# Kernel tuning notes

Hardware: AMD Instinct MI355X
Metric: run time of the kernel (lower is better)

The kernel has to match this reference:

```python
import jax, jax.numpy as jnp
import numpy as np

B, L, H = 32, 1024, 384


def setup_inputs() -> dict:
    key = jax.random.key(0)
    k1, k2 = jax.random.split(key)
    encoder_hidden_states = jax.random.normal(k1, (B, L, H), dtype=jnp.float32)
    durations_gt = jax.random.randint(k2, (B, L), 0, 8, dtype=jnp.int32)
    return {"encoder_hidden_states": encoder_hidden_states, "durations_gt": durations_gt}


def reference(encoder_hidden_states, durations_gt):
    # cumulative end-frame of each phoneme: [B, L]
    cum = jnp.cumsum(durations_gt, axis=1)
    total = cum[:, -1]                      # [B] expanded length per batch item
    T = int(jnp.max(total))                 # max expanded length (data-dependent)
    t = jnp.arange(T, dtype=cum.dtype)      # [T] output frame positions
    # source phoneme index for each output frame: number of cum entries <= t
    idx = jax.vmap(lambda c: jnp.searchsorted(c, t, side="right"))(cum)  # [B, T]
    idx = jnp.minimum(idx, L - 1)
    mask = (t[None, :] < total[:, None]).astype(jnp.float32)             # [B, T]
    # gather hidden states and zero out the padded tail
    out = jnp.take_along_axis(encoder_hidden_states, idx[:, :, None], axis=1)
    out = out * mask[:, :, None]
    return out, mask
```

## Files before the change

### kernel.cpp

```cpp
#include <hip/hip_runtime.h>

#define BB 32
#define LL 1024
#define HH 384
#define H4 (HH / 4)
#define TT 64
#define NT 256

__global__ __launch_bounds__(NT) void lenreg_kernel(
    const float* __restrict__ ehs,
    const int* __restrict__ dur,
    float* __restrict__ out,
    float* __restrict__ mask,
    int T)
{
    __shared__ int scum[LL];
    __shared__ int psum[NT];
    __shared__ int sidx[TT];

    const int tid = threadIdx.x;
    const int b   = blockIdx.y;
    const int t0  = blockIdx.x * TT;

    int4 d = ((const int4*)(dur + (size_t)b * LL))[tid];
    int p0 = d.x;
    int p1 = p0 + d.y;
    int p2 = p1 + d.z;
    int p3 = p2 + d.w;
    psum[tid] = p3;
    __syncthreads();
    #pragma unroll
    for (int off = 1; off < NT; off <<= 1) {
        int v = (tid >= off) ? psum[tid - off] : 0;
        __syncthreads();
        psum[tid] += v;
        __syncthreads();
    }
    const int excl = (tid > 0) ? psum[tid - 1] : 0;
    scum[4 * tid + 0] = excl + p0;
    scum[4 * tid + 1] = excl + p1;
    scum[4 * tid + 2] = excl + p2;
    scum[4 * tid + 3] = excl + p3;
    __syncthreads();

    const int total = scum[LL - 1];

    if (tid < TT) {
        const int t = t0 + tid;
        int lo = 0, hi = LL;
        while (lo < hi) {
            const int mid = (lo + hi) >> 1;
            if (scum[mid] <= t) lo = mid + 1; else hi = mid;
        }
        sidx[tid] = (lo < LL - 1) ? lo : (LL - 1);
        if (t < T) mask[(size_t)b * T + t] = (t < total) ? 1.0f : 0.0f;
    }
    __syncthreads();

    const float4* __restrict__ src_base = (const float4*)(ehs + (size_t)b * LL * HH);
    float4* __restrict__ out4 = (float4*)out;
    const float4 zero4 = make_float4(0.f, 0.f, 0.f, 0.f);

    for (int w = tid; w < TT * H4; w += NT) {
        const int tl = w / H4;
        const int v  = w - tl * H4;
        const int t  = t0 + tl;
        if (t >= T) break;
        float4 val = zero4;
        if (t < total) {
            val = src_base[(size_t)sidx[tl] * H4 + v];
        }
        out4[((size_t)b * T + t) * H4 + v] = val;
    }
}

extern "C" void kernel_launch(void* const* d_in, const int* in_sizes, int n_in,
                              void* d_out, int out_size, void* d_ws, size_t ws_size,
                              hipStream_t stream) {
    const float* ehs = (const float*)d_in[0];
    const int*   dur = (const int*)d_in[1];

    const int T = out_size / (BB * (HH + 1));

    float* out  = (float*)d_out;
    float* mask = (float*)d_out + (size_t)BB * T * HH;

    dim3 grid((T + TT - 1) / TT, BB);
    dim3 block(NT);
    lenreg_kernel<<<grid, block, 0, stream>>>(ehs, dur, out, mask, T);
}
```

Measured before the change: 229.2 us.

## Split prefix scan into separate kernel and double frames per block

Moves the per-batch cumulative sum of durations into a small pre-pass kernel that writes the scan to workspace. The gather blocks then load the precomputed cumulative array instead of redoing the scan in every block. The frame tile per block is also doubled, so there are fewer blocks and each one does more copying. The cost is an extra kernel launch and a global round-trip for the cumulative array.

```diff
diff --git a/kernel.cpp b/kernel.cpp
--- a/kernel.cpp
+++ b/kernel.cpp
@@ -4,43 +4,55 @@
 #define LL 1024
 #define HH 384
 #define H4 (HH / 4)
-#define TT 64
+#define TT 128
 #define NT 256
 
-__global__ __launch_bounds__(NT) void lenreg_kernel(
+__global__ __launch_bounds__(NT) void scan_kernel(
+    const int* __restrict__ dur,
+    int* __restrict__ cum)
+{
+    __shared__ int psum[NT];
+    const int tid = threadIdx.x;
+    const int b   = blockIdx.x;
+
+    int4 d = ((const int4*)(dur + (size_t)b * LL))[tid];
+    const int p0 = d.x;
+    const int p1 = p0 + d.y;
+    const int p2 = p1 + d.z;
+    const int p3 = p2 + d.w;
+    psum[tid] = p3;
+    __syncthreads();
+    #pragma unroll
+    for (int off = 1; off < NT; off <<= 1) {
+        const int v = (tid >= off) ? psum[tid - off] : 0;
+        __syncthreads();
+        psum[tid] += v;
+        __syncthreads();
+    }
+    const int excl = (tid > 0) ? psum[tid - 1] : 0;
+    int4 o;
+    o.x = excl + p0;
+    o.y = excl + p1;
+    o.z = excl + p2;
+    o.w = excl + p3;
+    ((int4*)(cum + (size_t)b * LL))[tid] = o;
+}
+
+__global__ __launch_bounds__(NT) void gather_kernel(
     const float* __restrict__ ehs,
-    const int* __restrict__ dur,
+    const int* __restrict__ cum,
     float* __restrict__ out,
     float* __restrict__ mask,
     int T)
 {
     __shared__ int scum[LL];
-    __shared__ int psum[NT];
     __shared__ int sidx[TT];
 
     const int tid = threadIdx.x;
     const int b   = blockIdx.y;
     const int t0  = blockIdx.x * TT;
 
-    int4 d = ((const int4*)(dur + (size_t)b * LL))[tid];
-    int p0 = d.x;
-    int p1 = p0 + d.y;
-    int p2 = p1 + d.z;
-    int p3 = p2 + d.w;
-    psum[tid] = p3;
-    __syncthreads();
-    #pragma unroll
-    for (int off = 1; off < NT; off <<= 1) {
-        int v = (tid >= off) ? psum[tid - off] : 0;
-        __syncthreads();
-        psum[tid] += v;
-        __syncthreads();
-    }
-    const int excl = (tid > 0) ? psum[tid - 1] : 0;
-    scum[4 * tid + 0] = excl + p0;
-    scum[4 * tid + 1] = excl + p1;
-    scum[4 * tid + 2] = excl + p2;
-    scum[4 * tid + 3] = excl + p3;
+    ((int4*)scum)[tid] = ((const int4*)(cum + (size_t)b * LL))[tid];
     __syncthreads();
 
     const int total = scum[LL - 1];
@@ -84,8 +96,10 @@
 
     float* out  = (float*)d_out;
     float* mask = (float*)d_out + (size_t)BB * T * HH;
+    int*   cum  = (int*)d_ws;
+
+    scan_kernel<<<dim3(BB), dim3(NT), 0, stream>>>(dur, cum);
 
     dim3 grid((T + TT - 1) / TT, BB);
-    dim3 block(NT);
-    lenreg_kernel<<<grid, block, 0, stream>>>(ehs, dur, out, mask, T);
+    gather_kernel<<<grid, dim3(NT), 0, stream>>>(ehs, cum, out, mask, T);
 }
```

Result: slower. 235.6 us (+2.8%).
